# Performance work log

Measured on AMD Instinct MI355X. Metric: run time of the kernel, lower is better.

## Reference

```python
import jax, jax.numpy as jnp
import numpy as np

SELECT_CHANNELS = 256


def _channel_stats(x):
    # x: [B, C, H, W] -> stats stacked over compressions (std, median, max): [3, B, C]
    std = jnp.std(x, axis=(2, 3))
    med = jnp.median(x, axis=(2, 3))
    mx = jnp.max(x, axis=(2, 3))
    return jnp.stack([std, med, mx], axis=0)


def setup_inputs() -> dict:
    key = jax.random.key(0)
    kx, k1, k2, k3, k4 = jax.random.split(key, 5)
    B, C, H, W = 8, 512, 128, 128
    F = 2  # probas_channels_factor
    Hdim = C * F
    S = 3  # number of compressions (std, median, max)
    x = jax.random.normal(kx, (B, C, H, W), dtype=jnp.float32)
    # Per-compression two-layer MLP (SE-style channel attention)
    W1 = jax.random.normal(k1, (S, C, Hdim), dtype=jnp.float32) * (1.0 / np.sqrt(C))
    b1 = jnp.zeros((S, Hdim), dtype=jnp.float32)
    W2 = jax.random.normal(k2, (S, Hdim, C), dtype=jnp.float32) * (1.0 / np.sqrt(Hdim))
    b2 = jnp.zeros((S, C), dtype=jnp.float32)
    return {"x": x, "W1": W1, "b1": b1, "W2": W2, "b2": b2}


def reference(x, W1, b1, W2, b2):
    # Channel-wise attention probabilities (probas_only=True, reduce_mean=True)
    stats = _channel_stats(x)                                   # [S, B, C]
    h = jax.nn.relu(jnp.einsum('sbc,sch->sbh', stats, W1) + b1[:, None, :])
    logits = jnp.einsum('sbh,shc->sbc', h, W2) + b2[:, None, :]  # [S, B, C]
    probs = jax.nn.softmax(jnp.mean(logits, axis=0), axis=-1)    # [B, C]
    # top-k channel selection + gather of full spatial maps
    _, top_idx = jax.lax.top_k(probs, SELECT_CHANNELS)           # [B, K]
    selected = jnp.take_along_axis(x, top_idx[:, :, None, None], axis=1)  # [B, K, H, W]
    return selected
```

## Files before the change

### kernel.cpp

```cpp
#include <hip/hip_runtime.h>
#include <math.h>

#define BATCH 8
#define CH 512
#define HW 16384
#define NS 3
#define HD 1024
#define KSEL 256


__device__ inline float key_to_float(unsigned int key) {
    unsigned int u = (key & 0x80000000u) ? (key ^ 0x80000000u) : ~key;
    return __uint_as_float(u);
}

__global__ __launch_bounds__(256) void stats_kernel(const float* __restrict__ x,
                                                    double* __restrict__ stats) {
    const int row = blockIdx.x;
    const int t = threadIdx.x;
    const int lane = t & 63, wid = t >> 6;

    __shared__ unsigned int hist[16 * 257];
    __shared__ unsigned int cnt[256];
    __shared__ double s_red[3][4];
    __shared__ unsigned int s_prefix, s_rank;
    __shared__ int s_cntle[4];
    __shared__ unsigned int s_mgt[4];

    const float4* xr = (const float4*)(x + (size_t)row * HW);

    unsigned int kv[64];
    double sum = 0.0, sumsq = 0.0;
    float mx = -INFINITY;

    #pragma unroll
    for (int i = 0; i < 16; ++i) {
        float4 f = xr[i * 256 + t];
        float c0 = f.x, c1 = f.y, c2 = f.z, c3 = f.w;
        sum += (double)c0 + (double)c1 + (double)c2 + (double)c3;
        sumsq += (double)c0 * (double)c0 + (double)c1 * (double)c1
               + (double)c2 * (double)c2 + (double)c3 * (double)c3;
        mx = fmaxf(mx, fmaxf(fmaxf(c0, c1), fmaxf(c2, c3)));
        unsigned int u0 = __float_as_uint(c0);
        unsigned int u1 = __float_as_uint(c1);
        unsigned int u2 = __float_as_uint(c2);
        unsigned int u3 = __float_as_uint(c3);
        kv[i * 4 + 0] = u0 ^ ((u0 & 0x80000000u) ? 0xFFFFFFFFu : 0x80000000u);
        kv[i * 4 + 1] = u1 ^ ((u1 & 0x80000000u) ? 0xFFFFFFFFu : 0x80000000u);
        kv[i * 4 + 2] = u2 ^ ((u2 & 0x80000000u) ? 0xFFFFFFFFu : 0x80000000u);
        kv[i * 4 + 3] = u3 ^ ((u3 & 0x80000000u) ? 0xFFFFFFFFu : 0x80000000u);
    }

    #pragma unroll
    for (int off = 32; off; off >>= 1) {
        sum += __shfl_down(sum, off);
        sumsq += __shfl_down(sumsq, off);
        float o = __shfl_down(mx, off);
        mx = fmaxf(mx, o);
    }
    if (lane == 0) { s_red[0][wid] = sum; s_red[1][wid] = sumsq; s_red[2][wid] = (double)mx; }

    unsigned int prefix = 0;
    int rank = 8191;
    unsigned int* myh = &hist[(t & 15) * 257];

    for (int p = 0; p < 4; ++p) {
        const int shift = 24 - 8 * p;
        for (int i = t; i < 16 * 257; i += 256) hist[i] = 0;
        __syncthreads();
        const unsigned int himask = (p == 0) ? 0u : (0xFFFFFFFFu << (32 - 8 * p));
        #pragma unroll
        for (int i = 0; i < 64; ++i) {
            unsigned int key = kv[i];
            if ((key & himask) == prefix) atomicAdd(&myh[(key >> shift) & 255], 1u);
        }
        __syncthreads();
        if (t < 256) {
            unsigned int c = 0;
            #pragma unroll
            for (int h = 0; h < 16; ++h) c += hist[h * 257 + t];
            cnt[t] = c;
        }
        __syncthreads();
        if (t == 0) {
            int r = rank;
            unsigned int b = 0;
            for (b = 0; b < 256; ++b) {
                unsigned int c = cnt[b];
                if ((unsigned int)r < c) break;
                r -= (int)c;
            }
            s_prefix = prefix | (b << shift);
            s_rank = (unsigned int)r;
        }
        __syncthreads();
        prefix = s_prefix;
        rank = (int)s_rank;
        __syncthreads();
    }

    const unsigned int k1 = prefix;

    int cntle = 0;
    unsigned int mgt = 0xFFFFFFFFu;
    #pragma unroll
    for (int i = 0; i < 64; ++i) {
        unsigned int key = kv[i];
        if (key <= k1) cntle++;
        else if (key < mgt) mgt = key;
    }
    #pragma unroll
    for (int off = 32; off; off >>= 1) {
        cntle += __shfl_down(cntle, off);
        unsigned int o = __shfl_down(mgt, off);
        if (o < mgt) mgt = o;
    }
    if (lane == 0) { s_cntle[wid] = cntle; s_mgt[wid] = mgt; }
    __syncthreads();

    if (t == 0) {
        double sum_t = s_red[0][0] + s_red[0][1] + s_red[0][2] + s_red[0][3];
        double sq_t  = s_red[1][0] + s_red[1][1] + s_red[1][2] + s_red[1][3];
        double mx_t = fmax(fmax(s_red[2][0], s_red[2][1]), fmax(s_red[2][2], s_red[2][3]));
        int cle = s_cntle[0] + s_cntle[1] + s_cntle[2] + s_cntle[3];
        unsigned int mg = s_mgt[0];
        if (s_mgt[1] < mg) mg = s_mgt[1];
        if (s_mgt[2] < mg) mg = s_mgt[2];
        if (s_mgt[3] < mg) mg = s_mgt[3];

        unsigned int k2 = (cle >= 8193) ? k1 : mg;
        double med = 0.5 * ((double)key_to_float(k1) + (double)key_to_float(k2));
        double mean = sum_t / (double)HW;
        double var = sq_t / (double)HW - mean * mean;
        if (var < 0.0) var = 0.0;

        stats[0 * (BATCH * CH) + row] = sqrt(var);
        stats[1 * (BATCH * CH) + row] = med;
        stats[2 * (BATCH * CH) + row] = mx_t;
    }
}

__global__ __launch_bounds__(256) void mlp1_kernel(const double* __restrict__ stats,
                                                   const float* __restrict__ W1,
                                                   const float* __restrict__ b1,
                                                   double* __restrict__ h) {
    const int bid = blockIdx.x;
    const int jc = bid & 3, sb = bid >> 2;
    const int s = sb >> 3, b = sb & 7;
    const int t = threadIdx.x;
    const int j = jc * 256 + t;

    __shared__ double st[CH];
    st[t] = stats[s * (BATCH * CH) + b * CH + t];
    st[t + 256] = stats[s * (BATCH * CH) + b * CH + t + 256];
    __syncthreads();

    double acc = (double)b1[s * HD + j];
    const float* w = W1 + (size_t)s * CH * HD + j;
    for (int c = 0; c < CH; ++c) acc += st[c] * (double)w[(size_t)c * HD];
    h[(size_t)sb * HD + j] = acc > 0.0 ? acc : 0.0;
}

__global__ __launch_bounds__(256) void mlp2_kernel(const double* __restrict__ h,
                                                   const float* __restrict__ W2,
                                                   const float* __restrict__ b2,
                                                   double* __restrict__ logits) {
    const int bid = blockIdx.x;
    const int cc = bid & 1, sb = bid >> 1;
    const int s = sb >> 3;
    const int t = threadIdx.x;
    const int c = cc * 256 + t;

    __shared__ double hh[HD];
    #pragma unroll
    for (int i = 0; i < 4; ++i) hh[t + i * 256] = h[(size_t)sb * HD + t + i * 256];
    __syncthreads();

    double acc = (double)b2[s * CH + c];
    const float* w = W2 + (size_t)s * HD * CH + c;
    for (int j = 0; j < HD; ++j) acc += hh[j] * (double)w[(size_t)j * CH];
    logits[(size_t)sb * CH + c] = acc;
}

__global__ __launch_bounds__(512) void rank_kernel(const double* __restrict__ logits,
                                                   int* __restrict__ sel) {
    const int b = blockIdx.x, t = threadIdx.x;
    __shared__ double L[CH];
    L[t] = logits[(0 * BATCH + b) * CH + t]
         + logits[(1 * BATCH + b) * CH + t]
         + logits[(2 * BATCH + b) * CH + t];
    __syncthreads();
    const double Li = L[t];
    int rank = 0;
    for (int j = 0; j < CH; ++j) {
        double Lj = L[j];
        rank += (Lj > Li) || (Lj == Li && j < t);
    }
    if (rank < KSEL) sel[b * KSEL + rank] = t;
}

__global__ __launch_bounds__(256) void gather_kernel(const float* __restrict__ x,
                                                     const int* __restrict__ sel,
                                                     float* __restrict__ out) {
    const int blk = blockIdx.x;
    const int b = blk >> 8;
    const int ch = sel[blk];
    const float4* src = (const float4*)(x + ((size_t)b * CH + ch) * HW);
    float4* dst = (float4*)(out + (size_t)blk * HW);
    const int t = threadIdx.x;
    #pragma unroll
    for (int i = 0; i < 16; ++i) dst[i * 256 + t] = src[i * 256 + t];
}

extern "C" void kernel_launch(void* const* d_in, const int* in_sizes, int n_in,
                              void* d_out, int out_size, void* d_ws, size_t ws_size,
                              hipStream_t stream) {
    const float* x  = (const float*)d_in[0];
    const float* W1 = (const float*)d_in[1];
    const float* b1 = (const float*)d_in[2];
    const float* W2 = (const float*)d_in[3];
    const float* b2 = (const float*)d_in[4];
    float* out = (float*)d_out;

    char* ws = (char*)d_ws;
    double* stats  = (double*)(ws);
    double* h      = (double*)(ws + 98304);
    double* logits = (double*)(ws + 98304 + 196608);
    int*    sel    = (int*)   (ws + 98304 + 196608 + 98304);

    stats_kernel<<<BATCH * CH, 256, 0, stream>>>(x, stats);
    mlp1_kernel<<<NS * BATCH * 4, 256, 0, stream>>>(stats, W1, b1, h);
    mlp2_kernel<<<NS * BATCH * 2, 256, 0, stream>>>(h, W2, b2, logits);
    rank_kernel<<<BATCH, 512, 0, stream>>>(logits, sel);
    gather_kernel<<<BATCH * KSEL, 256, 0, stream>>>(x, sel, out);
}
```

Baseline: 635.2 us.

## Split MLP reductions across more blocks with partial sums fused into consumers

The two MLP layers are split along their reduction dimension: layer 1 into 4 channel chunks and layer 2 into 8 hidden chunks, which multiplies the block count so the GPU is better filled. Each block writes partial sums to workspace. The bias add and ReLU move into the next kernel's load, and the logit partial sums plus b2 are combined in the rank kernel. The stats kernel also gets a min-blocks-per-CU hint of 4 in its launch bounds, which may limit registers for its 64-entry key array. The cost is extra partial-sum memory traffic and a change in double-precision summation order.

```diff
diff --git a/kernel.cpp b/kernel.cpp
--- a/kernel.cpp
+++ b/kernel.cpp
@@ -7,6 +7,8 @@
 #define NS 3
 #define HD 1024
 #define KSEL 256
+#define CSPLIT 4
+#define HSPLIT 8
 
 
 __device__ inline float key_to_float(unsigned int key) {
@@ -14,8 +16,8 @@
     return __uint_as_float(u);
 }
 
-__global__ __launch_bounds__(256) void stats_kernel(const float* __restrict__ x,
-                                                    double* __restrict__ stats) {
+__global__ __launch_bounds__(256, 4) void stats_kernel(const float* __restrict__ x,
+                                                       double* __restrict__ stats) {
     const int row = blockIdx.x;
     const int t = threadIdx.x;
     const int lane = t & 63, wid = t >> 6;
@@ -142,53 +144,78 @@
 
 __global__ __launch_bounds__(256) void mlp1_kernel(const double* __restrict__ stats,
                                                    const float* __restrict__ W1,
+                                                   double* __restrict__ hpart) {
+    const int bid = blockIdx.x;
+    const int jc = bid & 3;
+    const int sb = (bid >> 2) % (NS * BATCH);
+    const int cc = bid / (4 * NS * BATCH);
+    const int s = sb / BATCH, b = sb % BATCH;
+    const int t = threadIdx.x;
+    const int j = jc * 256 + t;
+
+    __shared__ double st[128];
+    if (t < 128) st[t] = stats[s * (BATCH * CH) + b * CH + cc * 128 + t];
+    __syncthreads();
+
+    double a0 = 0.0, a1 = 0.0;
+    const float* w = W1 + (size_t)s * CH * HD + (size_t)(cc * 128) * HD + j;
+    #pragma unroll 4
+    for (int c = 0; c < 128; c += 2) {
+        a0 += st[c]     * (double)w[(size_t)c * HD];
+        a1 += st[c + 1] * (double)w[(size_t)(c + 1) * HD];
+    }
+    hpart[((size_t)cc * (NS * BATCH) + sb) * HD + j] = a0 + a1;
+}
+
+__global__ __launch_bounds__(256) void mlp2_kernel(const double* __restrict__ hpart,
                                                    const float* __restrict__ b1,
-                                                   double* __restrict__ h) {
+                                                   const float* __restrict__ W2,
+                                                   double* __restrict__ lpart) {
     const int bid = blockIdx.x;
-    const int jc = bid & 3, sb = bid >> 2;
-    const int s = sb >> 3, b = sb & 7;
-    const int t = threadIdx.x;
-    const int j = jc * 256 + t;
-
-    __shared__ double st[CH];
-    st[t] = stats[s * (BATCH * CH) + b * CH + t];
-    st[t + 256] = stats[s * (BATCH * CH) + b * CH + t + 256];
-    __syncthreads();
-
-    double acc = (double)b1[s * HD + j];
-    const float* w = W1 + (size_t)s * CH * HD + j;
-    for (int c = 0; c < CH; ++c) acc += st[c] * (double)w[(size_t)c * HD];
-    h[(size_t)sb * HD + j] = acc > 0.0 ? acc : 0.0;
-}
-
-__global__ __launch_bounds__(256) void mlp2_kernel(const double* __restrict__ h,
-                                                   const float* __restrict__ W2,
+    const int cq = bid & 1;
+    const int sb = (bid >> 1) % (NS * BATCH);
+    const int hc = bid / (2 * NS * BATCH);
+    const int s = sb / BATCH;
+    const int t = threadIdx.x;
+    const int c = cq * 256 + t;
+
+    __shared__ double hh[128];
+    if (t < 128) {
+        const int j = hc * 128 + t;
+        double v = (double)b1[s * HD + j];
+        #pragma unroll
+        for (int cc = 0; cc < CSPLIT; ++cc)
+            v += hpart[((size_t)cc * (NS * BATCH) + sb) * HD + j];
+        hh[t] = v > 0.0 ? v : 0.0;
+    }
+    __syncthreads();
+
+    double a0 = 0.0, a1 = 0.0;
+    const float* w = W2 + (size_t)s * HD * CH + (size_t)(hc * 128) * CH + c;
+    #pragma unroll 4
+    for (int h = 0; h < 128; h += 2) {
+        a0 += hh[h]     * (double)w[(size_t)h * CH];
+        a1 += hh[h + 1] * (double)w[(size_t)(h + 1) * CH];
+    }
+    lpart[((size_t)hc * (NS * BATCH) + sb) * CH + c] = a0 + a1;
+}
+
+__global__ __launch_bounds__(512) void rank_kernel(const double* __restrict__ lpart,
                                                    const float* __restrict__ b2,
-                                                   double* __restrict__ logits) {
-    const int bid = blockIdx.x;
-    const int cc = bid & 1, sb = bid >> 1;
-    const int s = sb >> 3;
-    const int t = threadIdx.x;
-    const int c = cc * 256 + t;
-
-    __shared__ double hh[HD];
-    #pragma unroll
-    for (int i = 0; i < 4; ++i) hh[t + i * 256] = h[(size_t)sb * HD + t + i * 256];
-    __syncthreads();
-
-    double acc = (double)b2[s * CH + c];
-    const float* w = W2 + (size_t)s * HD * CH + c;
-    for (int j = 0; j < HD; ++j) acc += hh[j] * (double)w[(size_t)j * CH];
-    logits[(size_t)sb * CH + c] = acc;
-}
-
-__global__ __launch_bounds__(512) void rank_kernel(const double* __restrict__ logits,
                                                    int* __restrict__ sel) {
     const int b = blockIdx.x, t = threadIdx.x;
     __shared__ double L[CH];
-    L[t] = logits[(0 * BATCH + b) * CH + t]
-         + logits[(1 * BATCH + b) * CH + t]
-         + logits[(2 * BATCH + b) * CH + t];
+    double v = 0.0;
+    #pragma unroll
+    for (int s = 0; s < NS; ++s) {
+        double vs = (double)b2[s * CH + t];
+        const int sb = s * BATCH + b;
+        #pragma unroll
+        for (int hc = 0; hc < HSPLIT; ++hc)
+            vs += lpart[((size_t)hc * (NS * BATCH) + sb) * CH + t];
+        v += vs;
+    }
+    L[t] = v;
     __syncthreads();
     const double Li = L[t];
     int rank = 0;
@@ -224,13 +251,13 @@
 
     char* ws = (char*)d_ws;
     double* stats  = (double*)(ws);
-    double* h      = (double*)(ws + 98304);
-    double* logits = (double*)(ws + 98304 + 196608);
-    int*    sel    = (int*)   (ws + 98304 + 196608 + 98304);
+    double* hpart  = (double*)(ws + (96 << 10));
+    double* lpart  = (double*)(ws + (96 << 10) + (768 << 10));
+    int*    sel    = (int*)   (ws + (96 << 10) + (768 << 10) + (768 << 10));
 
     stats_kernel<<<BATCH * CH, 256, 0, stream>>>(x, stats);
-    mlp1_kernel<<<NS * BATCH * 4, 256, 0, stream>>>(stats, W1, b1, h);
-    mlp2_kernel<<<NS * BATCH * 2, 256, 0, stream>>>(h, W2, b2, logits);
-    rank_kernel<<<BATCH, 512, 0, stream>>>(logits, sel);
+    mlp1_kernel<<<CSPLIT * NS * BATCH * 4, 256, 0, stream>>>(stats, W1, hpart);
+    mlp2_kernel<<<HSPLIT * NS * BATCH * 2, 256, 0, stream>>>(hpart, b1, W2, lpart);
+    rank_kernel<<<BATCH, 512, 0, stream>>>(lpart, b2, sel);
     gather_kernel<<<BATCH * KSEL, 256, 0, stream>>>(x, sel, out);
 }
```

Measured after the change: 574.9 us. 9.5% less time.
